# Kernel optimization log

Measured on AMD Instinct MI355X. Metric: run time of the kernel, lower is better.

Reference implementation:

```python
import jax, jax.numpy as jnp
import numpy as np

B, S, D, H, SPAN = 4, 1024, 768, 12, 512
HD = D // H  # 64


def setup_inputs() -> dict:
    key = jax.random.key(0)
    ks = jax.random.split(key, 8)
    hidden_states = jax.random.normal(ks[0], (B, S, D), jnp.float32)
    rel_embeddings = jax.random.normal(ks[1], (2 * SPAN, D), jnp.float32) * 0.02
    Wq = jax.random.normal(ks[2], (D, D), jnp.float32) * 0.02
    Wk = jax.random.normal(ks[3], (D, D), jnp.float32) * 0.02
    Wv = jax.random.normal(ks[4], (D, D), jnp.float32) * 0.02
    Wo = jax.random.normal(ks[5], (D, D), jnp.float32) * 0.02
    bq = jnp.zeros((D,), jnp.float32); bk = jnp.zeros((D,), jnp.float32)
    bv = jnp.zeros((D,), jnp.float32); bo = jnp.zeros((D,), jnp.float32)
    ln_g = jnp.ones((D,), jnp.float32); ln_b = jnp.zeros((D,), jnp.float32)
    idx = jnp.arange(S)
    relative_pos = (idx[:, None] - idx[None, :]).astype(jnp.int32)  # q - k
    lengths = jnp.array([1024, 896, 768, 512])  # padding-style mask
    valid = idx[None, :] < lengths[:, None]  # [B,S]
    attention_mask = (valid[:, :, None] & valid[:, None, :])[:, None, :, :].astype(jnp.int32)  # [B,1,S,S]
    return dict(hidden_states=hidden_states, rel_embeddings=rel_embeddings,
                Wq=Wq, bq=bq, Wk=Wk, bk=bk, Wv=Wv, bv=bv, Wo=Wo, bo=bo,
                ln_g=ln_g, ln_b=ln_b, attention_mask=attention_mask,
                relative_pos=relative_pos)


def reference(hidden_states, rel_embeddings, Wq, bq, Wk, bk, Wv, bv, Wo, bo,
              ln_g, ln_b, attention_mask, relative_pos):
    # content projections -> [B,H,S,HD]
    q = (hidden_states @ Wq.T + bq).reshape(B, S, H, HD).transpose(0, 2, 1, 3)
    k = (hidden_states @ Wk.T + bk).reshape(B, S, H, HD).transpose(0, 2, 1, 3)
    v = (hidden_states @ Wv.T + bv).reshape(B, S, H, HD).transpose(0, 2, 1, 3)

    scale_qk = jnp.sqrt(jnp.float32(HD * 3))  # scale_factor = 3
    scores = jnp.einsum('bhqd,bhkd->bhqk', q, k) / scale_qk

    # shared-key position projections -> [H, 2*SPAN, HD]
    pos_q = (rel_embeddings @ Wq.T + bq).reshape(2 * SPAN, H, HD).transpose(1, 0, 2)
    pos_k = (rel_embeddings @ Wk.T + bk).reshape(2 * SPAN, H, HD).transpose(1, 0, 2)

    rp = relative_pos.astype(jnp.int32)
    # c2p: query vs relative key-position embedding, gathered by clamp(rel+span)
    c2p_att = jnp.einsum('bhqd,hkd->bhqk', q, pos_k)  # [B,H,S,2*SPAN]
    c2p_pos = jnp.clip(rp + SPAN, 0, 2 * SPAN - 1)
    c2p_idx = jnp.broadcast_to(c2p_pos[None, None], (B, H, S, S))
    c2p = jnp.take_along_axis(c2p_att, c2p_idx, axis=-1) / scale_qk

    # p2c: key vs relative query-position embedding, gathered by clamp(-rel+span), then transposed
    p2c_att = jnp.einsum('bhkd,hqd->bhkq', k, pos_q)  # [B,H,S,2*SPAN]
    p2c_pos = jnp.clip(SPAN - rp, 0, 2 * SPAN - 1)
    p2c_idx = jnp.broadcast_to(p2c_pos[None, None], (B, H, S, S))
    p2c = jnp.swapaxes(jnp.take_along_axis(p2c_att, p2c_idx, axis=-1), -1, -2)
    p2c = p2c / jnp.sqrt(jnp.float32(HD))  # note: torch uses sqrt(d) here, no scale_factor

    scores = scores + c2p + p2c

    # XSoftmax: masked softmax with zeros at masked positions
    mask = attention_mask.astype(bool)  # [B,1,S,S]
    neg = jnp.finfo(scores.dtype).min
    probs = jax.nn.softmax(jnp.where(mask, scores, neg), axis=-1)
    probs = jnp.where(mask, probs, jnp.float32(0))

    ctx = jnp.einsum('bhqk,bhkd->bhqd', probs, v).transpose(0, 2, 1, 3).reshape(B, S, D)

    # DebertaV2SelfOutput: dense + residual + LayerNorm(eps=1e-7)
    x = ctx @ Wo.T + bo + hidden_states
    mu = x.mean(-1, keepdims=True)
    var = ((x - mu) ** 2).mean(-1, keepdims=True)
    return (x - mu) / jnp.sqrt(var + 1e-7) * ln_g + ln_b
```

## Files before the change

kernel.cpp:

```cpp
#include <hip/hip_runtime.h>
#include <hip/hip_bf16.h>
#include <stdint.h>

typedef __hip_bfloat16 bf16;
typedef __attribute__((ext_vector_type(8))) short s8v;
typedef __attribute__((ext_vector_type(4))) float f4v;

__device__ __align__(16) bf16 g_hidden[4096 * 768];
__device__ __align__(16) bf16 g_rel[1024 * 768];
__device__ __align__(16) bf16 g_Wqkv[2304 * 768];
__device__ __align__(16) bf16 g_Wo[768 * 768];
__device__ __align__(16) bf16 g_biasQKV[2304];
__device__ __align__(16) bf16 g_biasPos[1536];
__device__ __align__(16) bf16 g_bo[768];
__device__ __align__(16) bf16 g_lng[768];
__device__ __align__(16) bf16 g_lnb[768];
__device__ __align__(16) bf16 g_Y1[4096 * 1536];
__device__ __align__(16) bf16 g_VT[48u * 64 * 1024];
__device__ __align__(16) bf16 g_Yp[1024 * 1536];
__device__ __align__(16) bf16 g_C2P[48u * 1024 * 1024];
__device__ __align__(16) bf16 g_P2C[48u * 1024 * 1024];
__device__ __align__(16) bf16 g_ctx[4096 * 768];
__device__ __align__(16) float g_X[4096 * 768];
__device__ int g_vq[4096], g_vk[4096], g_kmax[4];

__device__ __forceinline__ float bfs(short x) {
  return __uint_as_float(((unsigned int)(unsigned short)x) << 16);
}
__device__ __forceinline__ unsigned short f2bf(float f) {
  bf16 h = __float2bfloat16(f);
  return *(unsigned short*)&h;
}
__device__ __forceinline__ bool detect_bf16(const void* lng_raw) {
  return *(const unsigned int*)lng_raw == 0x3F803F80u;
}

__device__ __forceinline__ void cvt4(const void* src, bf16* dst, long grp, bool isbf) {
  long e = grp * 4;
  if (isbf) {
    *(uint2*)(dst + e) = *(const uint2*)((const bf16*)src + e);
  } else {
    float4 f = *(const float4*)((const float*)src + e);
    union { unsigned short us[4]; uint2 v; } u;
    u.us[0] = f2bf(f.x); u.us[1] = f2bf(f.y); u.us[2] = f2bf(f.z); u.us[3] = f2bf(f.w);
    *(uint2*)(dst + e) = u.v;
  }
}

__global__ __launch_bounds__(256) void cvt_inputs(
    const void* h, const void* r,
    const void* wq, const void* wk, const void* wv, const void* wo,
    const void* bq, const void* bk, const void* bv, const void* bo,
    const void* lg, const void* lb)
{
  if (blockIdx.x == 0 && threadIdx.x < 4) g_kmax[threadIdx.x] = 0;
  const bool isbf = detect_bf16(lg);
  long i = (long)blockIdx.x * 256 + threadIdx.x;
  if (i < 786432) { cvt4(h,  g_hidden,          i, isbf); return; } i -= 786432;
  if (i < 196608) { cvt4(r,  g_rel,             i, isbf); return; } i -= 196608;
  if (i < 147456) { cvt4(wq, g_Wqkv,            i, isbf); return; } i -= 147456;
  if (i < 147456) { cvt4(wk, g_Wqkv + 589824,   i, isbf); return; } i -= 147456;
  if (i < 147456) { cvt4(wv, g_Wqkv + 1179648,  i, isbf); return; } i -= 147456;
  if (i < 147456) { cvt4(wo, g_Wo,              i, isbf); return; } i -= 147456;
  if (i < 192)    { cvt4(bq, g_biasQKV,         i, isbf); return; } i -= 192;
  if (i < 192)    { cvt4(bk, g_biasQKV + 768,   i, isbf); return; } i -= 192;
  if (i < 192)    { cvt4(bv, g_biasQKV + 1536,  i, isbf); return; } i -= 192;
  if (i < 192)    { cvt4(bq, g_biasPos,         i, isbf); return; } i -= 192;
  if (i < 192)    { cvt4(bk, g_biasPos + 768,   i, isbf); return; } i -= 192;
  if (i < 192)    { cvt4(lg, g_lng,             i, isbf); return; } i -= 192;
  if (i < 192)    { cvt4(lb, g_lnb,             i, isbf); return; }
}

__global__ __launch_bounds__(256) void mask_prep(const int* __restrict__ mask) {
  int t = blockIdx.x * 256 + threadIdx.x;
  int b = t >> 10, i = t & 1023;
  int vq = mask[((size_t)(b * 1024 + i)) * 1024];
  int vk = mask[((size_t)(b * 1024)) * 1024 + i];
  g_vq[t] = vq;
  g_vk[t] = vk;
  if (vq | vk) atomicMax(&g_kmax[b], i + 1);
}

__global__ __launch_bounds__(256, 2) void gemm_bt(int which) {
  __shared__ short As[128][72];
  __shared__ short Bs[128][72];

  const bf16 *A, *B; const bf16* bias;
  int lda, ldb, K, mode;
  const int m0 = blockIdx.y * 128, n0 = blockIdx.x * 128;

  if (which == 0) {
    A = g_hidden; lda = 768; B = g_Wqkv; ldb = 768; bias = g_biasQKV; K = 768;
    mode = (n0 >= 1536) ? 5 : 0;
  } else if (which == 1) {
    A = g_rel; lda = 768; B = g_Wqkv; ldb = 768; bias = g_biasPos; K = 768; mode = 1;
  } else {
    A = g_ctx; lda = 768; B = g_Wo; ldb = 768; bias = g_bo; K = 768; mode = 4;
  }

  const int tid = threadIdx.x, wave = tid >> 6, lane = tid & 63;
  const int quad = lane >> 4, l15 = lane & 15;
  const int wm = (wave >> 1) * 64, wn = (wave & 1) * 64;
  const int sr = tid >> 2, sc8 = (tid & 3) * 16;

  f4v acc[4][4];
#pragma unroll
  for (int i = 0; i < 4; i++)
#pragma unroll
    for (int j = 0; j < 4; j++) acc[i][j] = (f4v){0.f, 0.f, 0.f, 0.f};

  uint4 pa0, pa1, pa2, pa3, pb0, pb1, pb2, pb3;
#define LOAD_T(k0)                                                           \
  {                                                                          \
    const bf16* ap = A + (size_t)(m0 + sr) * lda + (k0) + sc8;               \
    const bf16* ap2 = A + (size_t)(m0 + sr + 64) * lda + (k0) + sc8;         \
    const bf16* bp = B + (size_t)(n0 + sr) * ldb + (k0) + sc8;               \
    const bf16* bp2 = B + (size_t)(n0 + sr + 64) * ldb + (k0) + sc8;         \
    pa0 = *(const uint4*)ap;  pa1 = *(const uint4*)(ap + 8);                 \
    pa2 = *(const uint4*)ap2; pa3 = *(const uint4*)(ap2 + 8);                \
    pb0 = *(const uint4*)bp;  pb1 = *(const uint4*)(bp + 8);                 \
    pb2 = *(const uint4*)bp2; pb3 = *(const uint4*)(bp2 + 8);                \
  }

  LOAD_T(0)
  for (int k0 = 0; k0 < K; k0 += 64) {
    __syncthreads();
    *(uint4*)&As[sr][sc8] = pa0;      *(uint4*)&As[sr][sc8 + 8] = pa1;
    *(uint4*)&As[sr + 64][sc8] = pa2; *(uint4*)&As[sr + 64][sc8 + 8] = pa3;
    *(uint4*)&Bs[sr][sc8] = pb0;      *(uint4*)&Bs[sr][sc8 + 8] = pb1;
    *(uint4*)&Bs[sr + 64][sc8] = pb2; *(uint4*)&Bs[sr + 64][sc8 + 8] = pb3;
    if (k0 + 64 < K) LOAD_T(k0 + 64)
    __syncthreads();

    s8v af[4][2], bfr[4][2];
#pragma unroll
    for (int mt = 0; mt < 4; mt++) {
      af[mt][0] = *(const s8v*)&As[wm + mt * 16 + l15][quad * 8];
      af[mt][1] = *(const s8v*)&As[wm + mt * 16 + l15][32 + quad * 8];
    }
#pragma unroll
    for (int nt = 0; nt < 4; nt++) {
      bfr[nt][0] = *(const s8v*)&Bs[wn + nt * 16 + l15][quad * 8];
      bfr[nt][1] = *(const s8v*)&Bs[wn + nt * 16 + l15][32 + quad * 8];
    }
#pragma unroll
    for (int mt = 0; mt < 4; mt++)
#pragma unroll
      for (int nt = 0; nt < 4; nt++) {
        acc[mt][nt] = __builtin_amdgcn_mfma_f32_16x16x32_bf16(af[mt][0], bfr[nt][0], acc[mt][nt], 0, 0, 0);
        acc[mt][nt] = __builtin_amdgcn_mfma_f32_16x16x32_bf16(af[mt][1], bfr[nt][1], acc[mt][nt], 0, 0, 0);
      }
  }
#undef LOAD_T

  float biasv[4];
#pragma unroll
  for (int nt = 0; nt < 4; nt++)
    biasv[nt] = bfs(*(const short*)&bias[n0 + wn + nt * 16 + l15]);

#pragma unroll
  for (int mt = 0; mt < 4; mt++) {
#pragma unroll
    for (int nt = 0; nt < 4; nt++) {
      const int mbase = m0 + wm + mt * 16 + quad * 4;
      const int n = n0 + wn + nt * 16 + l15;
      if (mode == 5) {
        const int dd = n - 1536, hv = dd >> 6, hd = dd & 63;
        const int bb = mbase >> 10, ss = mbase & 1023;
        float t0 = acc[mt][nt][0] + biasv[nt], t1 = acc[mt][nt][1] + biasv[nt];
        float t2 = acc[mt][nt][2] + biasv[nt], t3 = acc[mt][nt][3] + biasv[nt];
        uint2 pk;
        pk.x = (unsigned int)f2bf(t0) | ((unsigned int)f2bf(t1) << 16);
        pk.y = (unsigned int)f2bf(t2) | ((unsigned int)f2bf(t3) << 16);
        *(uint2*)(g_VT + (((size_t)(bb * 12 + hv) * 64 + hd) << 10) + ss) = pk;
        continue;
      }
#pragma unroll
      for (int reg = 0; reg < 4; reg++) {
        const int m = mbase + reg;
        float v = acc[mt][nt][reg] + biasv[nt];
        if (mode == 0) {
          g_Y1[(size_t)m * 1536 + n] = __float2bfloat16(v);
        } else if (mode == 1) {
          g_Yp[(size_t)m * 1536 + n] = __float2bfloat16(v);
        } else {
          v += bfs(*(const short*)&g_hidden[(size_t)m * 768 + n]);
          g_X[(size_t)m * 768 + n] = v;
        }
      }
    }
  }
}

__global__ __launch_bounds__(256, 2) void band_gemm() {
  const int z = blockIdx.z;
  const int which = z / 48, bh = z % 48;
  const int b = bh / 12, hh = bh - b * 12;
  const int m0 = blockIdx.y * 128, n0 = blockIdx.x * 128;
  const int kmax = g_kmax[b];
  if (m0 >= kmax) return;
  const int lo = max(0, m0 + 513 - kmax);
  const int hi = min(1023, m0 + 639);
  if (n0 + 127 < lo || n0 > hi) return;

  const bf16* A = g_Y1 + (size_t)(b * 1024) * 1536 + (which ? 768 : 0) + hh * 64;
  const bf16* Bp = g_Yp + (which ? 0 : 768) + hh * 64;
  bf16* Cp = (which ? g_P2C : g_C2P) + ((size_t)bh << 20);

  __shared__ short As[128][68], Bs[128][68];
  const int tid = threadIdx.x, wave = tid >> 6, lane = tid & 63;
  const int quad = lane >> 4, l15 = lane & 15;
  const int wm = (wave >> 1) * 64, wn = (wave & 1) * 64;
  const int sr = tid >> 2, sc = (tid & 3) * 16;

  {
    const bf16* a0 = A + (size_t)(m0 + sr) * 1536 + sc;
    const bf16* a1 = A + (size_t)(m0 + sr + 64) * 1536 + sc;
    const bf16* b0 = Bp + (size_t)(n0 + sr) * 1536 + sc;
    const bf16* b1 = Bp + (size_t)(n0 + sr + 64) * 1536 + sc;
    *(uint4*)&As[sr][sc]          = *(const uint4*)a0;
    *(uint4*)&As[sr][sc + 8]      = *(const uint4*)(a0 + 8);
    *(uint4*)&As[sr + 64][sc]     = *(const uint4*)a1;
    *(uint4*)&As[sr + 64][sc + 8] = *(const uint4*)(a1 + 8);
    *(uint4*)&Bs[sr][sc]          = *(const uint4*)b0;
    *(uint4*)&Bs[sr][sc + 8]      = *(const uint4*)(b0 + 8);
    *(uint4*)&Bs[sr + 64][sc]     = *(const uint4*)b1;
    *(uint4*)&Bs[sr + 64][sc + 8] = *(const uint4*)(b1 + 8);
  }
  __syncthreads();

  s8v af[4][2], bfr[4][2];
#pragma unroll
  for (int mt = 0; mt < 4; mt++) {
    af[mt][0] = *(const s8v*)&As[wm + mt * 16 + l15][quad * 8];
    af[mt][1] = *(const s8v*)&As[wm + mt * 16 + l15][32 + quad * 8];
  }
#pragma unroll
  for (int nt = 0; nt < 4; nt++) {
    bfr[nt][0] = *(const s8v*)&Bs[wn + nt * 16 + l15][quad * 8];
    bfr[nt][1] = *(const s8v*)&Bs[wn + nt * 16 + l15][32 + quad * 8];
  }

  f4v acc[4][4];
#pragma unroll
  for (int mt = 0; mt < 4; mt++)
#pragma unroll
    for (int nt = 0; nt < 4; nt++) {
      acc[mt][nt] = __builtin_amdgcn_mfma_f32_16x16x32_bf16(af[mt][0], bfr[nt][0], (f4v){0.f, 0.f, 0.f, 0.f}, 0, 0, 0);
      acc[mt][nt] = __builtin_amdgcn_mfma_f32_16x16x32_bf16(af[mt][1], bfr[nt][1], acc[mt][nt], 0, 0, 0);
    }

#pragma unroll
  for (int mt = 0; mt < 4; mt++)
#pragma unroll
    for (int nt = 0; nt < 4; nt++) {
      const int m = m0 + wm + mt * 16 + quad * 4;
      const int n = n0 + wn + nt * 16 + l15;
#pragma unroll
      for (int reg = 0; reg < 4; reg++)
        Cp[(size_t)(m + reg) * 1024 + n] = __float2bfloat16(acc[mt][nt][reg]);
    }
}

__global__ __launch_bounds__(256, 4) void attn_mfma() {
  const int bh = blockIdx.y, b = bh / 12, hh = bh - b * 12;
  const int q0 = blockIdx.x * 64;
  const int tid = threadIdx.x, wave = tid >> 6, lane = tid & 63;
  const int quad = lane >> 4, l15 = lane & 15;
  const int kmax = g_kmax[b];

  if (q0 >= kmax) {
    uint4 zz = {0u, 0u, 0u, 0u};
#pragma unroll
    for (int s = tid; s < 512; s += 256) {
      int r = s >> 3, cc = (s & 7) * 8;
      *(uint4*)(g_ctx + (size_t)(b * 1024 + q0 + r) * 768 + hh * 64 + cc) = zz;
    }
    return;
  }

  __shared__ short Ks[64][68], VTs[64][68], Pl[4][16][68];

  const size_t qrow = (size_t)(b * 1024 + q0 + wave * 16 + l15) * 1536 + hh * 64;
  const s8v qf0 = *(const s8v*)(g_Y1 + qrow + quad * 8);
  const s8v qf1 = *(const s8v*)(g_Y1 + qrow + 32 + quad * 8);

  int vqr[4];
#pragma unroll
  for (int reg = 0; reg < 4; reg++)
    vqr[reg] = g_vq[b * 1024 + q0 + wave * 16 + quad * 4 + reg];

  f4v accO[4];
#pragma unroll
  for (int dt = 0; dt < 4; dt++) accO[dt] = (f4v){0.f, 0.f, 0.f, 0.f};
  float psum[4] = {0.f, 0.f, 0.f, 0.f};

  const int sr = tid >> 2, sc8 = (tid & 3) * 16;
  const bf16* Kbase = g_Y1 + (size_t)(b * 1024) * 1536 + 768 + hh * 64;
  const bf16* Vbase = g_VT + ((size_t)bh << 16);
  const bf16* __restrict__ C2Pb = g_C2P + ((size_t)bh << 20);
  const bf16* __restrict__ P2Cb = g_P2C + ((size_t)bh << 20);
  const int qg = q0 + wave * 16 + quad * 4;

  uint4 rk0, rk1, rv0, rv1;
#define LOAD_A(k0)                                                         \
  {                                                                        \
    const bf16* kp = Kbase + (size_t)((k0) + sr) * 1536 + sc8;             \
    rk0 = *(const uint4*)kp; rk1 = *(const uint4*)(kp + 8);                \
    const bf16* vp = Vbase + ((size_t)sr << 10) + (k0) + sc8;              \
    rv0 = *(const uint4*)vp; rv1 = *(const uint4*)(vp + 8);                \
  }

  LOAD_A(0)
  const float r192 = 0.0721687836487032f;
  const float r64 = 0.125f;

  for (int k0 = 0; k0 < kmax; k0 += 64) {
    __syncthreads();
    *(uint4*)&Ks[sr][sc8] = rk0;   *(uint4*)&Ks[sr][sc8 + 8] = rk1;
    *(uint4*)&VTs[sr][sc8] = rv0;  *(uint4*)&VTs[sr][sc8 + 8] = rv1;

    short c2s[16], p2s[16];
#pragma unroll
    for (int nt = 0; nt < 4; nt++) {
      const int k = k0 + nt * 16 + l15;
#pragma unroll
      for (int reg = 0; reg < 4; reg++) {
        const int d = qg + reg - k;
        const int cc = min(max(d + 512, 0), 1023);
        const int cp = min(max(512 - d, 0), 1023);
        c2s[nt * 4 + reg] = *(const short*)(C2Pb + (((size_t)(qg + reg)) << 10) + cc);
        p2s[nt * 4 + reg] = *(const short*)(P2Cb + (((size_t)k) << 10) + cp);
      }
    }

    if (k0 + 64 < kmax) LOAD_A(k0 + 64)
    __syncthreads();

    f4v sacc[4];
#pragma unroll
    for (int nt = 0; nt < 4; nt++) {
      s8v kb0 = *(const s8v*)&Ks[nt * 16 + l15][quad * 8];
      s8v kb1 = *(const s8v*)&Ks[nt * 16 + l15][32 + quad * 8];
      sacc[nt] = __builtin_amdgcn_mfma_f32_16x16x32_bf16(qf0, kb0, (f4v){0.f, 0.f, 0.f, 0.f}, 0, 0, 0);
      sacc[nt] = __builtin_amdgcn_mfma_f32_16x16x32_bf16(qf1, kb1, sacc[nt], 0, 0, 0);
    }

    const bool tail = (k0 + 64 > kmax);
#pragma unroll
    for (int nt = 0; nt < 4; nt++) {
      const int kl = nt * 16 + l15;
#pragma unroll
      for (int reg = 0; reg < 4; reg++) {
        float c2 = bfs(c2s[nt * 4 + reg]);
        float p2 = bfs(p2s[nt * 4 + reg]);
        float sc = (sacc[nt][reg] + c2) * r192 + p2 * r64;
        float pe = __expf(fminf(sc, 60.f));
        if (tail && (k0 + kl >= kmax)) pe = 0.f;
        psum[reg] += pe;
        Pl[wave][quad * 4 + reg][kl] = (short)f2bf(pe);
      }
    }

    s8v pa0 = *(const s8v*)&Pl[wave][l15][quad * 8];
    s8v pa1 = *(const s8v*)&Pl[wave][l15][32 + quad * 8];
#pragma unroll
    for (int dt = 0; dt < 4; dt++) {
      s8v vb0 = *(const s8v*)&VTs[dt * 16 + l15][quad * 8];
      s8v vb1 = *(const s8v*)&VTs[dt * 16 + l15][32 + quad * 8];
      accO[dt] = __builtin_amdgcn_mfma_f32_16x16x32_bf16(pa0, vb0, accO[dt], 0, 0, 0);
      accO[dt] = __builtin_amdgcn_mfma_f32_16x16x32_bf16(pa1, vb1, accO[dt], 0, 0, 0);
    }
  }
#undef LOAD_A

#pragma unroll
  for (int off = 1; off < 16; off <<= 1)
#pragma unroll
    for (int reg = 0; reg < 4; reg++) psum[reg] += __shfl_xor(psum[reg], off);

  float inv[4];
#pragma unroll
  for (int reg = 0; reg < 4; reg++)
    inv[reg] = (vqr[reg] != 0 && psum[reg] > 0.f) ? 1.f / psum[reg] : 0.f;

#pragma unroll
  for (int dt = 0; dt < 4; dt++)
#pragma unroll
    for (int reg = 0; reg < 4; reg++) {
      float v = accO[dt][reg] * inv[reg];
      g_ctx[(size_t)(b * 1024 + q0 + wave * 16 + quad * 4 + reg) * 768 + hh * 64 + dt * 16 + l15] =
          __float2bfloat16(v);
    }
}

__global__ __launch_bounds__(256) void ln_kernel(const void* lng_raw, void* out) {
  const bool isbf = detect_bf16(lng_raw);
  const int row = blockIdx.x;
  const int tid = threadIdx.x;
  const float* xr = g_X + (size_t)row * 768;
  float x0 = xr[tid], x1 = xr[tid + 256], x2 = xr[tid + 512];
  float s = x0 + x1 + x2;
  float s2 = x0 * x0 + x1 * x1 + x2 * x2;
#pragma unroll
  for (int off = 32; off; off >>= 1) { s += __shfl_xor(s, off); s2 += __shfl_xor(s2, off); }
  __shared__ float red[2][4];
  int w = tid >> 6, ln = tid & 63;
  if (ln == 0) { red[0][w] = s; red[1][w] = s2; }
  __syncthreads();
  float ts = red[0][0] + red[0][1] + red[0][2] + red[0][3];
  float ts2 = red[1][0] + red[1][1] + red[1][2] + red[1][3];
  float mu = ts * (1.f / 768.f);
  float var = fmaxf(ts2 * (1.f / 768.f) - mu * mu, 0.f);
  float rstd = rsqrtf(var + 1e-7f);
#pragma unroll
  for (int q = 0; q < 3; q++) {
    int cidx = tid + q * 256;
    float xv = (q == 0) ? x0 : (q == 1 ? x1 : x2);
    float gg = bfs(*(const short*)&g_lng[cidx]);
    float bb = bfs(*(const short*)&g_lnb[cidx]);
    float val = (xv - mu) * rstd * gg + bb;
    if (isbf) ((bf16*)out)[(size_t)row * 768 + cidx] = __float2bfloat16(val);
    else      ((float*)out)[(size_t)row * 768 + cidx] = val;
  }
}

extern "C" void kernel_launch(void* const* d_in, const int* in_sizes, int n_in,
                              void* d_out, int out_size, void* d_ws, size_t ws_size,
                              hipStream_t stream) {
  const int* amask = (const int*)d_in[12];
  (void)d_ws; (void)ws_size; (void)in_sizes; (void)n_in; (void)out_size;

  cvt_inputs<<<dim3(6150), 256, 0, stream>>>(
      d_in[0], d_in[1], d_in[2], d_in[4], d_in[6], d_in[8],
      d_in[3], d_in[5], d_in[7], d_in[9], d_in[10], d_in[11]);
  mask_prep<<<dim3(16), 256, 0, stream>>>(amask);
  gemm_bt<<<dim3(18, 32, 1), 256, 0, stream>>>(0);
  gemm_bt<<<dim3(12, 8, 1), 256, 0, stream>>>(1);
  band_gemm<<<dim3(8, 8, 96), 256, 0, stream>>>();
  attn_mfma<<<dim3(16, 48), 256, 0, stream>>>();
  gemm_bt<<<dim3(6, 32, 1), 256, 0, stream>>>(4);
  ln_kernel<<<dim3(4096), 256, 0, stream>>>(d_in[10], d_out);
}
```

Baseline: 379.2 us.

## Store P2C band in diagonal-major layout for coalesced gathers in attention

The p2c band GEMM now stages its tile in shared memory and writes it out re-indexed by diagonal (relative offset), plus separate left/right clamp-edge vectors. The attention kernel can then read p2c values contiguously along k for a fixed 1023-q row instead of doing strided per-k-row gathers. A barrier in the generic GEMM loop is also moved ahead of the next prefetch. This adds shared memory and a scatter-style epilogue to the band GEMM, plus extra select logic in attention.

```diff
diff --git a/kernel.cpp b/kernel.cpp
--- a/kernel.cpp
+++ b/kernel.cpp
@@ -19,7 +19,9 @@
 __device__ __align__(16) bf16 g_VT[48u * 64 * 1024];
 __device__ __align__(16) bf16 g_Yp[1024 * 1536];
 __device__ __align__(16) bf16 g_C2P[48u * 1024 * 1024];
-__device__ __align__(16) bf16 g_P2C[48u * 1024 * 1024];
+__device__ __align__(16) bf16 g_P2Cd[48u * 1024 * 1024];
+__device__ __align__(16) bf16 g_p2cL[48 * 1024];
+__device__ __align__(16) bf16 g_p2cR[48 * 1024];
 __device__ __align__(16) bf16 g_ctx[4096 * 768];
 __device__ __align__(16) float g_X[4096 * 768];
 __device__ int g_vq[4096], g_vk[4096], g_kmax[4];
@@ -129,8 +131,8 @@
     *(uint4*)&As[sr + 64][sc8] = pa2; *(uint4*)&As[sr + 64][sc8 + 8] = pa3;
     *(uint4*)&Bs[sr][sc8] = pb0;      *(uint4*)&Bs[sr][sc8 + 8] = pb1;
     *(uint4*)&Bs[sr + 64][sc8] = pb2; *(uint4*)&Bs[sr + 64][sc8 + 8] = pb3;
+    __syncthreads();
     if (k0 + 64 < K) LOAD_T(k0 + 64)
-    __syncthreads();
 
     s8v af[4][2], bfr[4][2];
 #pragma unroll
@@ -205,9 +207,9 @@
 
   const bf16* A = g_Y1 + (size_t)(b * 1024) * 1536 + (which ? 768 : 0) + hh * 64;
   const bf16* Bp = g_Yp + (which ? 0 : 768) + hh * 64;
-  bf16* Cp = (which ? g_P2C : g_C2P) + ((size_t)bh << 20);
 
   __shared__ short As[128][68], Bs[128][68];
+  __shared__ short S[128][132];
   const int tid = threadIdx.x, wave = tid >> 6, lane = tid & 63;
   const int quad = lane >> 4, l15 = lane & 15;
   const int wm = (wave >> 1) * 64, wn = (wave & 1) * 64;
@@ -250,16 +252,46 @@
       acc[mt][nt] = __builtin_amdgcn_mfma_f32_16x16x32_bf16(af[mt][1], bfr[nt][1], acc[mt][nt], 0, 0, 0);
     }
 
+  if (which == 0) {
+    bf16* Cp = g_C2P + ((size_t)bh << 20);
+#pragma unroll
+    for (int mt = 0; mt < 4; mt++)
+#pragma unroll
+      for (int nt = 0; nt < 4; nt++) {
+        const int m = m0 + wm + mt * 16 + quad * 4;
+        const int n = n0 + wn + nt * 16 + l15;
+#pragma unroll
+        for (int reg = 0; reg < 4; reg++)
+          Cp[(size_t)(m + reg) * 1024 + n] = __float2bfloat16(acc[mt][nt][reg]);
+      }
+    return;
+  }
+
 #pragma unroll
   for (int mt = 0; mt < 4; mt++)
 #pragma unroll
-    for (int nt = 0; nt < 4; nt++) {
-      const int m = m0 + wm + mt * 16 + quad * 4;
-      const int n = n0 + wn + nt * 16 + l15;
+    for (int nt = 0; nt < 4; nt++)
 #pragma unroll
       for (int reg = 0; reg < 4; reg++)
-        Cp[(size_t)(m + reg) * 1024 + n] = __float2bfloat16(acc[mt][nt][reg]);
-    }
+        S[wm + mt * 16 + quad * 4 + reg][wn + nt * 16 + l15] =
+            (short)f2bf(acc[mt][nt][reg]);
+  __syncthreads();
+
+  if (n0 == 0 && tid < 128)
+    g_p2cL[bh * 1024 + m0 + tid] = *(bf16*)&S[tid][0];
+  if (n0 == 896 && tid < 128)
+    g_p2cR[bh * 1024 + m0 + tid] = *(bf16*)&S[tid][127];
+
+  bf16* Pd = g_P2Cd + ((size_t)bh << 20);
+  for (int s = wave; s < 255; s += 4) {
+    const int dl = s - 127;
+    const int r = (n0 - m0) + dl + 511;
+    if (r < 0 || r > 1023) continue;
+    const int mlo = max(0, -dl), mhi = min(127, 127 - dl);
+    bf16* dst = Pd + ((size_t)r << 10) + m0;
+    for (int i = mlo + lane; i <= mhi; i += 64)
+      dst[i] = *(bf16*)&S[i][i + dl];
+  }
 }
 
 __global__ __launch_bounds__(256, 4) void attn_mfma() {
@@ -299,7 +331,9 @@
   const bf16* Kbase = g_Y1 + (size_t)(b * 1024) * 1536 + 768 + hh * 64;
   const bf16* Vbase = g_VT + ((size_t)bh << 16);
   const bf16* __restrict__ C2Pb = g_C2P + ((size_t)bh << 20);
-  const bf16* __restrict__ P2Cb = g_P2C + ((size_t)bh << 20);
+  const bf16* __restrict__ P2Cdb = g_P2Cd + ((size_t)bh << 20);
+  const bf16* __restrict__ p2cLb = g_p2cL + bh * 1024;
+  const bf16* __restrict__ p2cRb = g_p2cR + bh * 1024;
   const int qg = q0 + wave * 16 + quad * 4;
 
   uint4 rk0, rk1, rv0, rv1;
@@ -320,17 +354,18 @@
     *(uint4*)&Ks[sr][sc8] = rk0;   *(uint4*)&Ks[sr][sc8 + 8] = rk1;
     *(uint4*)&VTs[sr][sc8] = rv0;  *(uint4*)&VTs[sr][sc8 + 8] = rv1;
 
-    short c2s[16], p2s[16];
+    short c2s[16], p2i[16], plv[4], prv[4];
 #pragma unroll
     for (int nt = 0; nt < 4; nt++) {
       const int k = k0 + nt * 16 + l15;
+      plv[nt] = *(const short*)(p2cLb + k);
+      prv[nt] = *(const short*)(p2cRb + k);
 #pragma unroll
       for (int reg = 0; reg < 4; reg++) {
-        const int d = qg + reg - k;
-        const int cc = min(max(d + 512, 0), 1023);
-        const int cp = min(max(512 - d, 0), 1023);
-        c2s[nt * 4 + reg] = *(const short*)(C2Pb + (((size_t)(qg + reg)) << 10) + cc);
-        p2s[nt * 4 + reg] = *(const short*)(P2Cb + (((size_t)k) << 10) + cp);
+        const int q = qg + reg;
+        const int cc = min(max(q - k + 512, 0), 1023);
+        c2s[nt * 4 + reg] = *(const short*)(C2Pb + (((size_t)q) << 10) + cc);
+        p2i[nt * 4 + reg] = *(const short*)(P2Cdb + (((size_t)(1023 - q)) << 10) + k);
       }
     }
 
@@ -352,9 +387,11 @@
       const int kl = nt * 16 + l15;
 #pragma unroll
       for (int reg = 0; reg < 4; reg++) {
+        const int q = qg + reg;
+        const int d2 = (k0 + kl) - q + 512;
+        short p2s = (d2 < 0) ? plv[nt] : ((d2 > 1023) ? prv[nt] : p2i[nt * 4 + reg]);
         float c2 = bfs(c2s[nt * 4 + reg]);
-        float p2 = bfs(p2s[nt * 4 + reg]);
-        float sc = (sacc[nt][reg] + c2) * r192 + p2 * r64;
+        float sc = (sacc[nt][reg] + c2) * r192 + bfs(p2s) * r64;
         float pe = __expf(fminf(sc, 60.f));
         if (tail && (k0 + kl >= kmax)) pe = 0.f;
         psum[reg] += pe;
```

Measured after the change: 428.0 us. +12.9%, slower.
